# Kernel tuning notes

Hardware: AMD Instinct MI355X
Metric: run time of the kernel (lower is better)

The kernel has to match this reference:

```python
import jax, jax.numpy as jnp
import numpy as np

N_NODES = 50000
N_EDGES = 400000
D_IN, D_HID, D_OUT = 512, 512, 256


def setup_inputs() -> dict:
    key = jax.random.key(0)
    k = jax.random.split(key, 6)
    x = jax.random.normal(k[0], (N_NODES, D_IN), dtype=jnp.float32)
    edge_index = jax.random.randint(k[1], (2, N_EDGES), 0, N_NODES, dtype=jnp.int64)
    # Glorot-ish init for the two GCNConv linear layers
    W1 = jax.random.normal(k[2], (D_IN, D_HID), dtype=jnp.float32) * (1.0 / np.sqrt(D_IN))
    b1 = jnp.zeros((D_HID,), dtype=jnp.float32)
    W2 = jax.random.normal(k[3], (D_HID, D_OUT), dtype=jnp.float32) * (1.0 / np.sqrt(D_HID))
    b2 = jnp.zeros((D_OUT,), dtype=jnp.float32)
    return {"x": x, "edge_index": edge_index, "W1": W1, "b1": b1, "W2": W2, "b2": b2}


def _gcn_conv(x, W, b, src, dst, norm, n):
    """PyG GCNConv: h = x W; out[i] = sum_{j->i} norm_e * h[j] + b.
    src/dst already include self-loops; norm = d^-1/2[src] * d^-1/2[dst]."""
    h = x @ W  # [n, d_out]
    msgs = h[src] * norm[:, None]  # gather + scale per edge
    agg = jnp.zeros((n, h.shape[1]), dtype=h.dtype).at[dst].add(msgs)  # scatter-add
    return agg + b


def reference(x, edge_index, W1, b1, W2, b2):
    n = x.shape[0]
    loop = jnp.arange(n, dtype=edge_index.dtype)
    src = jnp.concatenate([edge_index[0], loop])  # add self-loops
    dst = jnp.concatenate([edge_index[1], loop])
    # symmetric normalization on the self-loop-augmented graph
    deg = jnp.zeros((n,), dtype=x.dtype).at[dst].add(1.0)
    dinv = jnp.where(deg > 0, jax.lax.rsqrt(deg), 0.0)
    norm = dinv[src] * dinv[dst]
    h = jax.nn.relu(_gcn_conv(x, W1, b1, src, dst, norm, n))
    return _gcn_conv(h, W2, b2, src, dst, norm, n)
```

## Files before the change

### kernel.cpp

```cpp
#include <hip/hip_runtime.h>
#include <stdint.h>

typedef __bf16 bf16_t;
typedef __bf16 bf16x8 __attribute__((ext_vector_type(8)));
typedef float f32x4 __attribute__((ext_vector_type(4)));
typedef uint32_t u32x4 __attribute__((ext_vector_type(4)));

#define N_NODES  50000
#define N_EDGES  400000
#define D_IN     512
#define D_HID    512
#define D_OUTD   256
#define M_PAD    50048
#define NB_SCAN  196

__device__ __forceinline__ uint32_t f2bf_bits(float x){
    uint32_t u = __float_as_uint(x);
    return (u + 0x7fffu + ((u >> 16) & 1u)) >> 16;
}
__device__ __forceinline__ void unpack8(uint4 v, float* f){
    f[0]=__uint_as_float(v.x<<16); f[1]=__uint_as_float(v.x & 0xffff0000u);
    f[2]=__uint_as_float(v.y<<16); f[3]=__uint_as_float(v.y & 0xffff0000u);
    f[4]=__uint_as_float(v.z<<16); f[5]=__uint_as_float(v.z & 0xffff0000u);
    f[6]=__uint_as_float(v.w<<16); f[7]=__uint_as_float(v.w & 0xffff0000u);
}
__device__ __forceinline__ void glds16(const bf16_t* g, bf16_t* l){
    __builtin_amdgcn_global_load_lds(
        (const __attribute__((address_space(1))) uint32_t*)g,
        (__attribute__((address_space(3))) uint32_t*)l, 16, 0, 0);
}

__global__ __launch_bounds__(256)
void conv_x_bf16(const float* __restrict__ x, bf16_t* __restrict__ Xb,
                 int* __restrict__ deg){
    const int t = blockIdx.x * 256 + threadIdx.x;
    if (t < N_NODES) deg[t] = 1;
    const int row = t >> 7;
    uint2 o;
    if (row < N_NODES){
        f32x4 v = __builtin_nontemporal_load(((const f32x4*)x) + t);
        o.x = f2bf_bits(v.x) | (f2bf_bits(v.y) << 16);
        o.y = f2bf_bits(v.z) | (f2bf_bits(v.w) << 16);
    } else { o.x = 0u; o.y = 0u; }
    ((uint2*)Xb)[t] = o;
}

__global__ __launch_bounds__(256)
void conv_w_both(const float* __restrict__ W1, const float* __restrict__ W2,
                 bf16_t* __restrict__ W1t, bf16_t* __restrict__ W2t,
                 const int* __restrict__ ei, int* __restrict__ deg){
    const int idx = blockIdx.x * 256 + threadIdx.x;
    if (idx < N_EDGES) atomicAdd(&deg[ei[N_EDGES + idx]], 1);
    const int n = idx >> 9;
    const int k = idx & 511;
    if (n < 512) W1t[idx] = (bf16_t)W1[k * 512 + n];
    else if (n < 768) W2t[(n - 512) * 512 + k] = (bf16_t)W2[k * 256 + (n - 512)];
}

__global__ __launch_bounds__(256)
void k_scan_dinv(const int* __restrict__ deg, float* __restrict__ dinv,
                 int* __restrict__ part, int* __restrict__ bsum, int n){
    __shared__ int tmp[256];
    int i = blockIdx.x*256 + threadIdx.x;
    int d = (i < n) ? deg[i] : 1;
    if (i < n) dinv[i] = rsqrtf((float)d);
    int v = (i < n) ? (d - 1) : 0;
    tmp[threadIdx.x] = v;
    __syncthreads();
    for (int off = 1; off < 256; off <<= 1){
        int t = (threadIdx.x >= off) ? tmp[threadIdx.x - off] : 0;
        __syncthreads();
        tmp[threadIdx.x] += t;
        __syncthreads();
    }
    if (i < n) part[i] = tmp[threadIdx.x] - v;
    if (threadIdx.x == 255) bsum[blockIdx.x] = tmp[255];
}
__global__ __launch_bounds__(256)
void k_scan_bsum(const int* __restrict__ bsum, int* __restrict__ bsum2, int nb){
    __shared__ int tmp[256];
    int v = (threadIdx.x < nb) ? bsum[threadIdx.x] : 0;
    tmp[threadIdx.x] = v;
    __syncthreads();
    for (int off = 1; off < 256; off <<= 1){
        int t = (threadIdx.x >= off) ? tmp[threadIdx.x - off] : 0;
        __syncthreads();
        tmp[threadIdx.x] += t;
        __syncthreads();
    }
    if (threadIdx.x < nb) bsum2[threadIdx.x] = tmp[threadIdx.x] - v;
}
__global__ __launch_bounds__(256)
void k_finalize_rowptr(const int* __restrict__ part, const int* __restrict__ bsum2,
                       int* __restrict__ rowp, int* __restrict__ cursor, int n){
    int i = blockIdx.x*256 + threadIdx.x;
    if (i < n){ int r = part[i] + bsum2[blockIdx.x]; rowp[i] = r; cursor[i] = r; }
    if (i == 0) rowp[n] = N_EDGES;
}
__global__ __launch_bounds__(256)
void k_place(const int* __restrict__ ei, const float* __restrict__ dinv,
             int* __restrict__ cursor, int* __restrict__ csrc, float* __restrict__ cnorm){
    int e = blockIdx.x*256 + threadIdx.x;
    if (e < N_EDGES){
        int s = ei[e];
        int d = ei[N_EDGES + e];
        int p = atomicAdd(&cursor[d], 1);
        csrc[p]  = s;
        cnorm[p] = dinv[s] * dinv[d];
    }
}

__global__ __launch_bounds__(256, 2)
void gemm_bf16_mfma(const bf16_t* __restrict__ A, const bf16_t* __restrict__ Bt,
                    bf16_t* __restrict__ C, int N, int K)
{
    __shared__ bf16_t As[2][128*64];
    __shared__ bf16_t Bs[2][128*64];

    const int tid  = threadIdx.x;
    const int wave = tid >> 6;
    const int lane = tid & 63;
    const int wr = wave >> 1;
    const int wc = wave & 1;
    const int mBase = blockIdx.x * 128;
    const int nBase = blockIdx.y * 128;

    const int sr = lane >> 3;
    const int sc = (lane & 7) ^ sr;
    const bf16_t* Asrc[4]; const bf16_t* Bsrc[4];
    #pragma unroll
    for (int r = 0; r < 4; ++r){
        const int row = r*32 + wave*8 + sr;
        Asrc[r] = A  + (size_t)(mBase + row) * K + sc*8;
        Bsrc[r] = Bt + (size_t)(nBase + row) * K + sc*8;
    }

    auto stage = [&](int k0, int p){
        bf16_t* Ad = &As[p][0];
        bf16_t* Bd = &Bs[p][0];
        #pragma unroll
        for (int r = 0; r < 4; ++r) glds16(Asrc[r] + k0, Ad + (r*256 + tid)*8);
        #pragma unroll
        for (int r = 0; r < 4; ++r) glds16(Bsrc[r] + k0, Bd + (r*256 + tid)*8);
    };

    const int m16 = lane & 15;
    const int q8  = (lane >> 4) << 3;
    const int swz = (m16 & 7) << 3;
    const int aBase = (wr*64 + m16)*64;
    const int bBase = (wc*64 + m16)*64;

    f32x4 acc[4][4] = {};

    stage(0, 0);
    const int KT = K >> 6;
    for (int kt = 0; kt < KT; ++kt){
        const int p = kt & 1;
        __builtin_amdgcn_s_barrier();
        __builtin_amdgcn_sched_barrier(0);
        if (kt + 1 < KT){
            stage((kt + 1) << 6, p ^ 1);
            asm volatile("s_waitcnt vmcnt(8)" ::: "memory");
        } else {
            asm volatile("s_waitcnt vmcnt(0)" ::: "memory");
        }
        __builtin_amdgcn_sched_barrier(0);
        __builtin_amdgcn_s_barrier();
        const bf16_t* Ab = &As[p][0];
        const bf16_t* Bb = &Bs[p][0];
        #pragma unroll
        for (int kk = 0; kk < 2; ++kk){
            const int ko = (kk*32 + q8) ^ swz;
            bf16x8 a[4], b[4];
            #pragma unroll
            for (int t = 0; t < 4; ++t){
                a[t] = *(const bf16x8*)(Ab + aBase + t*1024 + ko);
                b[t] = *(const bf16x8*)(Bb + bBase + t*1024 + ko);
            }
            #pragma unroll
            for (int i = 0; i < 4; ++i){
                #pragma unroll
                for (int j = 0; j < 4; ++j){
                    acc[i][j] = __builtin_amdgcn_mfma_f32_16x16x32_bf16(a[i], b[j], acc[i][j], 0, 0, 0);
                }
            }
        }
    }

    const int qr = lane >> 4;
    #pragma unroll
    for (int i = 0; i < 4; ++i){
        const int row0 = mBase + wr*64 + i*16 + qr*4;
        #pragma unroll
        for (int j = 0; j < 4; ++j){
            const int col = nBase + wc*64 + j*16 + m16;
            bf16_t* Cp = C + (size_t)row0 * N + col;
            #pragma unroll
            for (int r = 0; r < 4; ++r)
                Cp[(size_t)r * N] = (bf16_t)acc[i][j][r];
        }
    }
}

__global__ __launch_bounds__(256)
void agg_bias_relu_512(const bf16_t* __restrict__ T, const int* __restrict__ rowp,
                       const int* __restrict__ csrc, const float* __restrict__ cnorm,
                       const float* __restrict__ dinv, const float* __restrict__ bias,
                       bf16_t* __restrict__ H)
{
    const int gw   = (blockIdx.x * 256 + threadIdx.x) >> 6;
    const int lane = threadIdx.x & 63;
    if (gw >= N_NODES) return;
    const float di = dinv[gw];
    const uint4* Tr = (const uint4*)T;
    float acc[8];
    {
        uint4 v = Tr[(size_t)gw * 64 + lane];
        float f[8]; unpack8(v, f);
        const float w = di * di;
        #pragma unroll
        for (int j = 0; j < 8; ++j) acc[j] = w * f[j];
    }
    int e = rowp[gw];
    const int e1 = rowp[gw + 1];

    if (e + 4 <= e1){
        uint4 v0, v1, v2, v3; float w0, w1, w2, w3;
        {
            const int s0 = csrc[e], s1 = csrc[e+1], s2 = csrc[e+2], s3 = csrc[e+3];
            w0 = cnorm[e]; w1 = cnorm[e+1]; w2 = cnorm[e+2]; w3 = cnorm[e+3];
            v0 = Tr[(size_t)s0 * 64 + lane];
            v1 = Tr[(size_t)s1 * 64 + lane];
            v2 = Tr[(size_t)s2 * 64 + lane];
            v3 = Tr[(size_t)s3 * 64 + lane];
        }
        e += 4;
        for (; e + 4 <= e1; e += 4){
            const int   t0 = csrc[e],   t1 = csrc[e+1], t2 = csrc[e+2], t3 = csrc[e+3];
            const float x0 = cnorm[e],  x1 = cnorm[e+1], x2 = cnorm[e+2], x3 = cnorm[e+3];
            uint4 n0 = Tr[(size_t)t0 * 64 + lane];
            uint4 n1 = Tr[(size_t)t1 * 64 + lane];
            uint4 n2 = Tr[(size_t)t2 * 64 + lane];
            uint4 n3 = Tr[(size_t)t3 * 64 + lane];
            float f[8];
            unpack8(v0, f);
            #pragma unroll
            for (int j = 0; j < 8; ++j) acc[j] += w0 * f[j];
            unpack8(v1, f);
            #pragma unroll
            for (int j = 0; j < 8; ++j) acc[j] += w1 * f[j];
            unpack8(v2, f);
            #pragma unroll
            for (int j = 0; j < 8; ++j) acc[j] += w2 * f[j];
            unpack8(v3, f);
            #pragma unroll
            for (int j = 0; j < 8; ++j) acc[j] += w3 * f[j];
            v0 = n0; v1 = n1; v2 = n2; v3 = n3;
            w0 = x0; w1 = x1; w2 = x2; w3 = x3;
        }
        float f[8];
        unpack8(v0, f);
        #pragma unroll
        for (int j = 0; j < 8; ++j) acc[j] += w0 * f[j];
        unpack8(v1, f);
        #pragma unroll
        for (int j = 0; j < 8; ++j) acc[j] += w1 * f[j];
        unpack8(v2, f);
        #pragma unroll
        for (int j = 0; j < 8; ++j) acc[j] += w2 * f[j];
        unpack8(v3, f);
        #pragma unroll
        for (int j = 0; j < 8; ++j) acc[j] += w3 * f[j];
    }
    for (; e < e1; ++e){
        const int   s = csrc[e];
        const float w = cnorm[e];
        uint4 v = Tr[(size_t)s * 64 + lane];
        float f[8]; unpack8(v, f);
        #pragma unroll
        for (int j = 0; j < 8; ++j) acc[j] += w * f[j];
    }
    const float4 b0 = ((const float4*)bias)[lane*2];
    const float4 b1 = ((const float4*)bias)[lane*2 + 1];
    float r[8] = {acc[0]+b0.x, acc[1]+b0.y, acc[2]+b0.z, acc[3]+b0.w,
                  acc[4]+b1.x, acc[5]+b1.y, acc[6]+b1.z, acc[7]+b1.w};
    u32x4 o;
    o.x = f2bf_bits(fmaxf(r[0],0.f)) | (f2bf_bits(fmaxf(r[1],0.f)) << 16);
    o.y = f2bf_bits(fmaxf(r[2],0.f)) | (f2bf_bits(fmaxf(r[3],0.f)) << 16);
    o.z = f2bf_bits(fmaxf(r[4],0.f)) | (f2bf_bits(fmaxf(r[5],0.f)) << 16);
    o.w = f2bf_bits(fmaxf(r[6],0.f)) | (f2bf_bits(fmaxf(r[7],0.f)) << 16);
    __builtin_nontemporal_store(o, ((u32x4*)(H + (size_t)gw * 512)) + lane);
}

__global__ __launch_bounds__(256)
void agg_bias_out_256(const bf16_t* __restrict__ T, const int* __restrict__ rowp,
                      const int* __restrict__ csrc, const float* __restrict__ cnorm,
                      const float* __restrict__ dinv, const float* __restrict__ bias,
                      float* __restrict__ out)
{
    const int wid  = (blockIdx.x * 256 + threadIdx.x) >> 6;
    const int half = (threadIdx.x >> 5) & 1;
    const int l32  = threadIdx.x & 31;
    const int node = wid * 2 + half;
    if (node >= N_NODES) return;
    const float di = dinv[node];
    float acc[8];
    {
        uint4 v = ((const uint4*)(T + (size_t)node * 256))[l32];
        float f[8]; unpack8(v, f);
        const float w = di * di;
        #pragma unroll
        for (int j = 0; j < 8; ++j) acc[j] = w * f[j];
    }
    int e = rowp[node];
    const int e1 = rowp[node + 1];
    for (; e + 4 <= e1; e += 4){
        const int   s0 = csrc[e],   s1 = csrc[e+1], s2 = csrc[e+2], s3 = csrc[e+3];
        const float w0 = cnorm[e],  w1 = cnorm[e+1], w2 = cnorm[e+2], w3 = cnorm[e+3];
        uint4 v0 = ((const uint4*)(T + (size_t)s0 * 256))[l32];
        uint4 v1 = ((const uint4*)(T + (size_t)s1 * 256))[l32];
        uint4 v2 = ((const uint4*)(T + (size_t)s2 * 256))[l32];
        uint4 v3 = ((const uint4*)(T + (size_t)s3 * 256))[l32];
        float f[8];
        unpack8(v0, f);
        #pragma unroll
        for (int j = 0; j < 8; ++j) acc[j] += w0 * f[j];
        unpack8(v1, f);
        #pragma unroll
        for (int j = 0; j < 8; ++j) acc[j] += w1 * f[j];
        unpack8(v2, f);
        #pragma unroll
        for (int j = 0; j < 8; ++j) acc[j] += w2 * f[j];
        unpack8(v3, f);
        #pragma unroll
        for (int j = 0; j < 8; ++j) acc[j] += w3 * f[j];
    }
    for (; e < e1; ++e){
        const int   s = csrc[e];
        const float w = cnorm[e];
        uint4 v = ((const uint4*)(T + (size_t)s * 256))[l32];
        float f[8]; unpack8(v, f);
        #pragma unroll
        for (int j = 0; j < 8; ++j) acc[j] += w * f[j];
    }
    const float4 b0 = ((const float4*)bias)[l32*2];
    const float4 b1 = ((const float4*)bias)[l32*2 + 1];
    f32x4 o0 = {acc[0]+b0.x, acc[1]+b0.y, acc[2]+b0.z, acc[3]+b0.w};
    f32x4 o1 = {acc[4]+b1.x, acc[5]+b1.y, acc[6]+b1.z, acc[7]+b1.w};
    __builtin_nontemporal_store(o0, ((f32x4*)(out + (size_t)node * 256)) + l32*2);
    __builtin_nontemporal_store(o1, ((f32x4*)(out + (size_t)node * 256)) + l32*2 + 1);
}

extern "C" void kernel_launch(void* const* d_in, const int* in_sizes, int n_in,
                              void* d_out, int out_size, void* d_ws, size_t ws_size,
                              hipStream_t stream)
{
    const float* x  = (const float*)d_in[0];
    const int*   ei = (const int*)d_in[1];
    const float* W1 = (const float*)d_in[2];
    const float* b1 = (const float*)d_in[3];
    const float* W2 = (const float*)d_in[4];
    const float* b2 = (const float*)d_in[5];
    float* out = (float*)d_out;

    char* w = (char*)d_ws;
    auto alloc = [&](size_t bytes) -> char* {
        char* p = w; w += (bytes + 255) & ~(size_t)255; return p;
    };
    bf16_t* Xb    = (bf16_t*)alloc((size_t)M_PAD * 512 * 2);
    bf16_t* T     = (bf16_t*)alloc((size_t)M_PAD * 512 * 2);
    bf16_t* W1t   = (bf16_t*)alloc(512 * 512 * 2);
    bf16_t* W2t   = (bf16_t*)alloc(256 * 512 * 2);
    int*    deg   = (int*)  alloc(N_NODES * 4);
    float*  dinv  = (float*)alloc(N_NODES * 4);
    int*    rowp  = (int*)  alloc((N_NODES + 1) * 4);
    int*    cursor= (int*)  alloc(N_NODES * 4);
    int*    part  = (int*)  alloc(N_NODES * 4);
    int*    bsum  = (int*)  alloc(NB_SCAN * 4);
    int*    bsum2 = (int*)  alloc(NB_SCAN * 4);
    int*    csrc  = (int*)  alloc(N_EDGES * 4);
    float*  cnorm = (float*)alloc(N_EDGES * 4);

    conv_x_bf16<<<(M_PAD*128)/256, 256, 0, stream>>>(x, Xb, deg);
    conv_w_both<<<1568, 256, 0, stream>>>(W1, W2, W1t, W2t, ei, deg);

    k_scan_dinv<<<NB_SCAN, 256, 0, stream>>>(deg, dinv, part, bsum, N_NODES);
    k_scan_bsum <<<1, 256, 0, stream>>>(bsum, bsum2, NB_SCAN);
    k_finalize_rowptr<<<NB_SCAN, 256, 0, stream>>>(part, bsum2, rowp, cursor, N_NODES);
    k_place   <<<(N_EDGES+255)/256, 256, 0, stream>>>(ei, dinv, cursor, csrc, cnorm);

    gemm_bf16_mfma<<<dim3(M_PAD/128, 512/128), 256, 0, stream>>>(Xb, W1t, T, 512, 512);
    agg_bias_relu_512<<<(N_NODES+3)/4, 256, 0, stream>>>(T, rowp, csrc, cnorm, dinv, b1, Xb);

    gemm_bf16_mfma<<<dim3(M_PAD/128, 256/128), 256, 0, stream>>>(Xb, W2t, T, 256, 512);
    agg_bias_out_256<<<(25000+3)/4, 256, 0, stream>>>(T, rowp, csrc, cnorm, dinv, b2, out);
}
```

Baseline: 400.0 us.

## Widen GEMM tile to 128x256 with single-buffered K=32 stages

Rewrites the bf16 MFMA GEMM to use 128x256 output tiles, so each wave holds a 4x8 accumulator grid, and halves the grid's N dimension. The double-buffered 64-wide K pipeline with the XOR-swizzled LDS layout is replaced by a single-buffered 32-wide K step, synchronised with __syncthreads. The aim is more reuse of each A tile and fewer blocks. In exchange it loses load/compute overlap, may introduce LDS bank conflicts now that the swizzle is gone, and raises register pressure under launch_bounds(256,2).

```diff
diff --git a/kernel.cpp b/kernel.cpp
--- a/kernel.cpp
+++ b/kernel.cpp
@@ -114,86 +114,61 @@
 void gemm_bf16_mfma(const bf16_t* __restrict__ A, const bf16_t* __restrict__ Bt,
                     bf16_t* __restrict__ C, int N, int K)
 {
-    __shared__ bf16_t As[2][128*64];
-    __shared__ bf16_t Bs[2][128*64];
+    __shared__ bf16_t As[128*32];
+    __shared__ bf16_t Bs[256*32];
 
     const int tid  = threadIdx.x;
+    const int lane = tid & 63;
     const int wave = tid >> 6;
-    const int lane = tid & 63;
     const int wr = wave >> 1;
     const int wc = wave & 1;
     const int mBase = blockIdx.x * 128;
-    const int nBase = blockIdx.y * 128;
-
-    const int sr = lane >> 3;
-    const int sc = (lane & 7) ^ sr;
-    const bf16_t* Asrc[4]; const bf16_t* Bsrc[4];
+    const int nBase = blockIdx.y * 256;
+
+    const int srow = tid >> 2;
+    const int scol = (tid & 3) << 3;
+    const bf16_t* Ag0 = A  + (size_t)(mBase + srow) * K + scol;
+    const bf16_t* Ag1 = A  + (size_t)(mBase + 64 + srow) * K + scol;
+    const bf16_t* Bg[4];
     #pragma unroll
-    for (int r = 0; r < 4; ++r){
-        const int row = r*32 + wave*8 + sr;
-        Asrc[r] = A  + (size_t)(mBase + row) * K + sc*8;
-        Bsrc[r] = Bt + (size_t)(nBase + row) * K + sc*8;
-    }
-
-    auto stage = [&](int k0, int p){
-        bf16_t* Ad = &As[p][0];
-        bf16_t* Bd = &Bs[p][0];
-        #pragma unroll
-        for (int r = 0; r < 4; ++r) glds16(Asrc[r] + k0, Ad + (r*256 + tid)*8);
-        #pragma unroll
-        for (int r = 0; r < 4; ++r) glds16(Bsrc[r] + k0, Bd + (r*256 + tid)*8);
-    };
+    for (int c = 0; c < 4; ++c)
+        Bg[c] = Bt + (size_t)(nBase + c*64 + srow) * K + scol;
 
     const int m16 = lane & 15;
-    const int q8  = (lane >> 4) << 3;
-    const int swz = (m16 & 7) << 3;
-    const int aBase = (wr*64 + m16)*64;
-    const int bBase = (wc*64 + m16)*64;
-
-    f32x4 acc[4][4] = {};
-
-    stage(0, 0);
-    const int KT = K >> 6;
-    for (int kt = 0; kt < KT; ++kt){
-        const int p = kt & 1;
-        __builtin_amdgcn_s_barrier();
-        __builtin_amdgcn_sched_barrier(0);
-        if (kt + 1 < KT){
-            stage((kt + 1) << 6, p ^ 1);
-            asm volatile("s_waitcnt vmcnt(8)" ::: "memory");
-        } else {
-            asm volatile("s_waitcnt vmcnt(0)" ::: "memory");
-        }
-        __builtin_amdgcn_sched_barrier(0);
-        __builtin_amdgcn_s_barrier();
-        const bf16_t* Ab = &As[p][0];
-        const bf16_t* Bb = &Bs[p][0];
-        #pragma unroll
-        for (int kk = 0; kk < 2; ++kk){
-            const int ko = (kk*32 + q8) ^ swz;
-            bf16x8 a[4], b[4];
-            #pragma unroll
-            for (int t = 0; t < 4; ++t){
-                a[t] = *(const bf16x8*)(Ab + aBase + t*1024 + ko);
-                b[t] = *(const bf16x8*)(Bb + bBase + t*1024 + ko);
-            }
-            #pragma unroll
-            for (int i = 0; i < 4; ++i){
-                #pragma unroll
-                for (int j = 0; j < 4; ++j){
-                    acc[i][j] = __builtin_amdgcn_mfma_f32_16x16x32_bf16(a[i], b[j], acc[i][j], 0, 0, 0);
-                }
+    const int q   = lane >> 4;
+    const bf16_t* aP = &As[(wr*64 + m16)*32 + q*8];
+    const bf16_t* bP = &Bs[(wc*128 + m16)*32 + q*8];
+
+    f32x4 acc[4][8] = {};
+
+    for (int k0 = 0; k0 < K; k0 += 32){
+        glds16(Ag0 + k0, &As[(size_t)tid * 8]);
+        glds16(Ag1 + k0, &As[(size_t)(256 + tid) * 8]);
+        #pragma unroll
+        for (int c = 0; c < 4; ++c)
+            glds16(Bg[c] + k0, &Bs[(size_t)(c*256 + tid) * 8]);
+        __syncthreads();
+        bf16x8 a[4], b[8];
+        #pragma unroll
+        for (int t = 0; t < 4; ++t) a[t] = *(const bf16x8*)(aP + t*16*32);
+        #pragma unroll
+        for (int t = 0; t < 8; ++t) b[t] = *(const bf16x8*)(bP + t*16*32);
+        #pragma unroll
+        for (int i = 0; i < 4; ++i){
+            #pragma unroll
+            for (int j = 0; j < 8; ++j){
+                acc[i][j] = __builtin_amdgcn_mfma_f32_16x16x32_bf16(a[i], b[j], acc[i][j], 0, 0, 0);
             }
         }
-    }
-
-    const int qr = lane >> 4;
+        __syncthreads();
+    }
+
     #pragma unroll
     for (int i = 0; i < 4; ++i){
-        const int row0 = mBase + wr*64 + i*16 + qr*4;
-        #pragma unroll
-        for (int j = 0; j < 4; ++j){
-            const int col = nBase + wc*64 + j*16 + m16;
+        const int row0 = mBase + wr*64 + i*16 + q*4;
+        #pragma unroll
+        for (int j = 0; j < 8; ++j){
+            const int col = nBase + wc*128 + j*16 + m16;
             bf16_t* Cp = C + (size_t)row0 * N + col;
             #pragma unroll
             for (int r = 0; r < 4; ++r)
@@ -389,9 +364,9 @@
     k_finalize_rowptr<<<NB_SCAN, 256, 0, stream>>>(part, bsum2, rowp, cursor, N_NODES);
     k_place   <<<(N_EDGES+255)/256, 256, 0, stream>>>(ei, dinv, cursor, csrc, cnorm);
 
-    gemm_bf16_mfma<<<dim3(M_PAD/128, 512/128), 256, 0, stream>>>(Xb, W1t, T, 512, 512);
+    gemm_bf16_mfma<<<dim3(M_PAD/128, 512/256), 256, 0, stream>>>(Xb, W1t, T, 512, 512);
     agg_bias_relu_512<<<(N_NODES+3)/4, 256, 0, stream>>>(T, rowp, csrc, cnorm, dinv, b1, Xb);
 
-    gemm_bf16_mfma<<<dim3(M_PAD/128, 256/128), 256, 0, stream>>>(Xb, W2t, T, 256, 512);
+    gemm_bf16_mfma<<<dim3(M_PAD/128, 256/256), 256, 0, stream>>>(Xb, W2t, T, 256, 512);
     agg_bias_out_256<<<(25000+3)/4, 256, 0, stream>>>(T, rowp, csrc, cnorm, dinv, b2, out);
 }
```

Result: no change. 392.5 us (-1.9%).
